# Kernel optimization log

Hardware: AMD Instinct MI355X
Metric: run time of the kernel (lower is better)

Reference implementation:

```python
import jax, jax.numpy as jnp
import numpy as np

N = 100000      # nodes
E = 600000      # edges
IN = 128        # in_dim
HID = 32        # hidden_dim per head (layer 1)
HEADS = 4       # num_heads (layer 1)
NEG_SLOPE = 0.2 # PyG GATConv default negative_slope


def setup_inputs() -> dict:
    key = jax.random.key(0)
    ks = jax.random.split(key, 10)
    x = jax.random.normal(ks[0], (N, IN), dtype=jnp.float32)
    edge_index = jax.random.randint(ks[1], (2, E), 0, N, dtype=jnp.int64)
    # layer 1 params: W1 [IN, HEADS*HID], attention vectors [HEADS, HID], bias [HEADS*HID]
    W1 = jax.random.normal(ks[2], (IN, HEADS * HID), dtype=jnp.float32) / np.float32(np.sqrt(IN))
    att_src1 = jax.random.normal(ks[3], (HEADS, HID), dtype=jnp.float32) * 0.1
    att_dst1 = jax.random.normal(ks[4], (HEADS, HID), dtype=jnp.float32) * 0.1
    b1 = jnp.zeros((HEADS * HID,), dtype=jnp.float32)
    # layer 2 params: heads=1, out channels=1, concat=False
    W2 = jax.random.normal(ks[5], (HEADS * HID, 1), dtype=jnp.float32) / np.float32(np.sqrt(HEADS * HID))
    att_src2 = jax.random.normal(ks[6], (1, 1), dtype=jnp.float32) * 0.1
    att_dst2 = jax.random.normal(ks[7], (1, 1), dtype=jnp.float32) * 0.1
    b2 = jnp.zeros((1,), dtype=jnp.float32)
    return {"x": x, "edge_index": edge_index, "W1": W1, "att_src1": att_src1,
            "att_dst1": att_dst1, "b1": b1, "W2": W2, "att_src2": att_src2,
            "att_dst2": att_dst2, "b2": b2}


def gat_layer(x, src, dst, W, a_src, a_dst, b, heads, ch, concat):
    """PyG GATConv (eval mode): edge score + segment softmax + scatter aggregate."""
    n = x.shape[0]
    h = (x @ W).reshape(n, heads, ch)                    # [N,H,C]
    e_src = jnp.einsum('nhc,hc->nh', h, a_src)           # alpha_src per node
    e_dst = jnp.einsum('nhc,hc->nh', h, a_dst)           # alpha_dst per node
    e = jax.nn.leaky_relu(e_src[src] + e_dst[dst], NEG_SLOPE)  # [E,H]
    m = jax.ops.segment_max(e, dst, num_segments=n)      # stable softmax per dst
    p = jnp.exp(e - m[dst])
    denom = jax.ops.segment_sum(p, dst, num_segments=n)
    alpha = p / (denom[dst] + 1e-16)                     # [E,H]
    out = jax.ops.segment_sum(alpha[:, :, None] * h[src], dst, num_segments=n)  # [N,H,C]
    out = out.reshape(n, heads * ch) if concat else out.mean(axis=1)
    return out + b


def reference(x, edge_index, W1, att_src1, att_dst1, b1, W2, att_src2, att_dst2, b2):
    n = x.shape[0]
    loops = jnp.arange(n, dtype=edge_index.dtype)        # PyG add_self_loops=True
    src = jnp.concatenate([edge_index[0], loops])
    dst = jnp.concatenate([edge_index[1], loops])
    h1 = gat_layer(x, src, dst, W1, att_src1, att_dst1, b1, HEADS, HID, True)   # [N, HEADS*HID]
    out = gat_layer(h1, src, dst, W2, att_src2, att_dst2, b2, 1, 1, False)      # [N, 1]
    return out
```

## Files before the change

kernel.cpp:

```cpp
#include <hip/hip_runtime.h>
#include <hip/hip_fp16.h>
#include <math.h>

#define N_NODES 100000
#define E_EDGES 600000
#define IN_DIM  128
#define HID     32
#define HEADS   4
#define NEG     0.2f
#define CAP     32

typedef __attribute__((ext_vector_type(8))) _Float16 f16x8;
typedef __attribute__((ext_vector_type(4))) float f32x4;

__device__ __forceinline__ float lrelu(float v) { return v > 0.f ? v : NEG * v; }

#define SWZ(r, byteoff) ((byteoff) ^ (((r) & 7) << 4))


__global__ __launch_bounds__(128) void wprep_kernel(const float* __restrict__ W1,
                                                    const float* __restrict__ as1,
                                                    const float* __restrict__ ad1,
                                                    __half* __restrict__ wtx,
                                                    int* __restrict__ cnt) {
    int tid = blockIdx.x * 128 + threadIdx.x;
    for (int i = tid; i < N_NODES; i += 144 * 128) cnt[i] = 0;

    int b = blockIdx.x;
    int t = threadIdx.x;
    float v;
    if (b < 128) {
        v = W1[t * 128 + b];
    } else if (b < 136) {
        int h = b - 128;
        int hh = h & 3;
        const float* av = (h < 4) ? (as1 + hh * 32) : (ad1 + hh * 32);
        float s = 0.f;
        #pragma unroll 8
        for (int c = 0; c < 32; ++c) s += W1[t * 128 + hh * 32 + c] * av[c];
        v = s;
    } else {
        v = 0.f;
    }
    wtx[b * 128 + t] = __float2half(v);
}


__global__ __launch_bounds__(256) void scatter_kernel(const int* __restrict__ ei,
                                                      int* __restrict__ cnt,
                                                      int* __restrict__ idxb) {
    int e = blockIdx.x * 256 + threadIdx.x;
    if (e < E_EDGES) {
        int d = ei[E_EDGES + e];
        int slot = atomicAdd(&cnt[d], 1);
        if (slot < CAP) idxb[d * CAP + slot] = ei[e];
    }
}


__global__ __launch_bounds__(256) void gemm1_kernel(const float* __restrict__ x,
                                                    const __half* __restrict__ wtx,
                                                    __half* __restrict__ h1h,
                                                    float* __restrict__ aab) {
    __shared__ __half lx[64 * 128];
    __shared__ __half lw[144 * 128];
    int t = threadIdx.x;
    int row0 = blockIdx.x * 64;

    #pragma unroll
    for (int it = 0; it < 9; ++it) {
        int idx = t + it * 256;
        int r = idx >> 4, c = idx & 15;
        uint4 v = ((const uint4*)wtx)[idx];
        *(uint4*)((char*)lw + SWZ(r, r * 256 + c * 16)) = v;
    }
    #pragma unroll
    for (int it = 0; it < 8; ++it) {
        int idx = t + it * 256;
        int r = idx >> 5, c = idx & 31;
        int gr = row0 + r;
        float4 v = make_float4(0.f, 0.f, 0.f, 0.f);
        if (gr < N_NODES) v = ((const float4*)x)[gr * 32 + c];
        union { uint2 u; __half2 h[2]; } pk;
        pk.h[0] = __floats2half2_rn(v.x, v.y);
        pk.h[1] = __floats2half2_rn(v.z, v.w);
        *(uint2*)((char*)lx + SWZ(r, r * 256 + c * 8)) = pk.u;
    }
    __syncthreads();

    int w = t >> 6, lane = t & 63;
    int li = lane & 15, g = lane >> 4;
    int arow = w * 16 + li;

    f16x8 af[4];
    #pragma unroll
    for (int kt = 0; kt < 4; ++kt)
        af[kt] = *(const f16x8*)((const char*)lx + SWZ(arow, arow * 256 + kt * 64 + g * 16));

    f32x4 acc[9];
    #pragma unroll
    for (int ct = 0; ct < 9; ++ct) acc[ct] = (f32x4){0.f, 0.f, 0.f, 0.f};

    #pragma unroll
    for (int ct = 0; ct < 9; ++ct) {
        int n = ct * 16 + li;
        #pragma unroll
        for (int kt = 0; kt < 4; ++kt) {
            f16x8 bf = *(const f16x8*)((const char*)lw + SWZ(n, n * 256 + kt * 64 + g * 16));
            acc[ct] = __builtin_amdgcn_mfma_f32_16x16x32_f16(af[kt], bf, acc[ct], 0, 0, 0);
        }
    }

    int gr0 = row0 + w * 16 + g * 4;
    #pragma unroll
    for (int ct = 0; ct < 8; ++ct) {
        int col = ct * 16 + li;
        #pragma unroll
        for (int q = 0; q < 4; ++q) {
            int gr = gr0 + q;
            if (gr < N_NODES) h1h[gr * 128 + col] = __float2half(acc[ct][q]);
        }
    }
    if (li < 8) {
        #pragma unroll
        for (int q = 0; q < 4; ++q) {
            int gr = gr0 + q;
            if (gr < N_NODES) aab[gr * 8 + li] = acc[8][q];
        }
    }
}


__global__ __launch_bounds__(256) void agg1_kernel(const __half* __restrict__ h1h,
                                                   const float* __restrict__ aab,
                                                   const int* __restrict__ cnt,
                                                   const int* __restrict__ idxb,
                                                   const float* __restrict__ b1,
                                                   const float* __restrict__ W2,
                                                   const float* __restrict__ att_src2,
                                                   const float* __restrict__ att_dst2,
                                                   float* __restrict__ h2,
                                                   float* __restrict__ a2s,
                                                   float* __restrict__ a2d) {
    int tid = threadIdx.x;
    int c = tid & 15;
    int n = blockIdx.x * 16 + (tid >> 4);
    int head = c >> 2;
    int deg = min(cnt[n], CAP);
    const int* nb = idxb + (size_t)n * CAP;
    float adn = aab[n * 8 + 4 + head];

    __half2 acc01 = __half2(0.f, 0.f), acc23 = acc01, acc45 = acc01, acc67 = acc01;
    float den = 0.f;

    int s = (deg > 0) ? nb[0] : 0;
    for (int e = 0; e < deg; ++e) {
        int s_next = nb[e + 1];
        float p = __expf(lrelu(aab[s * 8 + head] + adn));
        __half2 pp = __float2half2_rn(p);
        union { uint4 u; __half2 h[4]; } hv;
        hv.u = *(const uint4*)&h1h[s * 128 + c * 8];
        acc01 = __hfma2(pp, hv.h[0], acc01);
        acc23 = __hfma2(pp, hv.h[1], acc23);
        acc45 = __hfma2(pp, hv.h[2], acc45);
        acc67 = __hfma2(pp, hv.h[3], acc67);
        den += p;
        s = s_next;
    }

    float s0 = __low2float(acc01), s1 = __high2float(acc01);
    float s2 = __low2float(acc23), s3 = __high2float(acc23);
    float s4 = __low2float(acc45), s5 = __high2float(acc45);
    float s6 = __low2float(acc67), s7 = __high2float(acc67);

    {
        float p = __expf(lrelu(aab[n * 8 + head] + adn));
        union { uint4 u; __half2 h[4]; } hv;
        hv.u = *(const uint4*)&h1h[n * 128 + c * 8];
        float2 f0 = __half22float2(hv.h[0]), f1 = __half22float2(hv.h[1]);
        float2 f2 = __half22float2(hv.h[2]), f3 = __half22float2(hv.h[3]);
        s0 += p * f0.x; s1 += p * f0.y; s2 += p * f1.x; s3 += p * f1.y;
        s4 += p * f2.x; s5 += p * f2.y; s6 += p * f3.x; s7 += p * f3.y;
        den += p;
    }

    float inv = 1.f / (den + 1e-16f);
    float4 bv0 = ((const float4*)b1)[c * 2];
    float4 bv1 = ((const float4*)b1)[c * 2 + 1];
    float o0 = s0 * inv + bv0.x, o1 = s1 * inv + bv0.y;
    float o2 = s2 * inv + bv0.z, o3 = s3 * inv + bv0.w;
    float o4 = s4 * inv + bv1.x, o5 = s5 * inv + bv1.y;
    float o6 = s6 * inv + bv1.z, o7 = s7 * inv + bv1.w;

    float4 wv0 = ((const float4*)W2)[c * 2];
    float4 wv1 = ((const float4*)W2)[c * 2 + 1];
    float pp = o0 * wv0.x + o1 * wv0.y + o2 * wv0.z + o3 * wv0.w
             + o4 * wv1.x + o5 * wv1.y + o6 * wv1.z + o7 * wv1.w;
    #pragma unroll
    for (int m = 1; m <= 8; m <<= 1) pp += __shfl_xor(pp, m, 64);
    if (c == 0) {
        h2[n] = pp;
        a2s[n] = pp * att_src2[0];
        a2d[n] = pp * att_dst2[0];
    }
}


__global__ __launch_bounds__(256) void agg2_kernel(const float* __restrict__ h2,
                                                   const float* __restrict__ a2s,
                                                   const float* __restrict__ a2d,
                                                   const int* __restrict__ cnt,
                                                   const int* __restrict__ idxb,
                                                   const float* __restrict__ b2,
                                                   float* __restrict__ out) {
    int n = blockIdx.x * 256 + threadIdx.x;
    if (n >= N_NODES) return;
    float adn = a2d[n];
    int deg = min(cnt[n], CAP);
    const int* nb = idxb + (size_t)n * CAP;
    float num = 0.f, den = 0.f;
    for (int i = 0; i < deg; i += 4) {
        int s[4]; bool val[4]; float as_[4], hs[4];
        #pragma unroll
        for (int j = 0; j < 4; ++j) {
            val[j] = (i + j) < deg;
            s[j] = val[j] ? nb[i + j] : n;
        }
        #pragma unroll
        for (int j = 0; j < 4; ++j) as_[j] = a2s[s[j]];
        #pragma unroll
        for (int j = 0; j < 4; ++j) hs[j] = h2[s[j]];
        #pragma unroll
        for (int j = 0; j < 4; ++j) {
            float p = val[j] ? __expf(lrelu(as_[j] + adn)) : 0.f;
            num += p * hs[j];
            den += p;
        }
    }
    {
        float p = __expf(lrelu(a2s[n] + adn));
        num += p * h2[n];
        den += p;
    }
    out[n] = num / (den + 1e-16f) + b2[0];
}


extern "C" void kernel_launch(void* const* d_in, const int* in_sizes, int n_in,
                              void* d_out, int out_size, void* d_ws, size_t ws_size,
                              hipStream_t stream) {
    const float* x        = (const float*)d_in[0];
    const int*   ei       = (const int*)d_in[1];
    const float* W1       = (const float*)d_in[2];
    const float* att_src1 = (const float*)d_in[3];
    const float* att_dst1 = (const float*)d_in[4];
    const float* b1       = (const float*)d_in[5];
    const float* W2       = (const float*)d_in[6];
    const float* att_src2 = (const float*)d_in[7];
    const float* att_dst2 = (const float*)d_in[8];
    const float* b2       = (const float*)d_in[9];
    float* out = (float*)d_out;

    char* ws = (char*)d_ws;
    size_t off = 0;
    auto alloc = [&](size_t bytes) {
        char* p = ws + off;
        off = (off + bytes + 255) & ~(size_t)255;
        return p;
    };
    __half* h1h    = (__half*)alloc((size_t)N_NODES * 128 * 2);
    float*  aab    = (float*)alloc((size_t)N_NODES * 8 * 4);
    __half* wtx    = (__half*)alloc((size_t)144 * 128 * 2);
    float*  h2     = (float*)alloc((size_t)N_NODES * 4);
    float*  a2s    = (float*)alloc((size_t)N_NODES * 4);
    float*  a2d    = (float*)alloc((size_t)N_NODES * 4);
    int*    cnt    = (int*)alloc((size_t)N_NODES * 4);
    int*    idxb   = (int*)alloc(((size_t)N_NODES * CAP + 64) * 4);

    const int NB_NODE = (N_NODES + 255) / 256;
    const int NB_EDGE = (E_EDGES + 255) / 256;
    const int NB_AGG1 = N_NODES / 16;
    const int NB_GEMM = (N_NODES + 63) / 64;

    wprep_kernel<<<144, 128, 0, stream>>>(W1, att_src1, att_dst1, wtx, cnt);
    scatter_kernel<<<NB_EDGE, 256, 0, stream>>>(ei, cnt, idxb);
    gemm1_kernel<<<NB_GEMM, 256, 0, stream>>>(x, wtx, h1h, aab);
    agg1_kernel<<<NB_AGG1, 256, 0, stream>>>(h1h, aab, cnt, idxb,
                                             b1, W2, att_src2, att_dst2,
                                             h2, a2s, a2d);
    agg2_kernel<<<NB_NODE, 256, 0, stream>>>(h2, a2s, a2d, cnt, idxb, b2, out);
}
```

Before: 191.8 us.

## Fuse edge scatter into GEMM launch and pack layer-2 node data as float4

The edge-bucketing scatter runs as extra blocks of the GEMM kernel instead of a separate launch, so the memory-bound atomics can overlap with GEMM compute and one launch is removed. Layer-2 per-node values (h2, alpha_src, alpha_dst) are packed into one float4 array so agg2 does a single 16-byte gather per neighbour instead of two scalar gathers. In exchange, scatter blocks reserve the GEMM's large shared-memory allocation, which may limit how many fit per CU, and the packed array moves more bytes per node.

```diff
diff --git a/kernel.cpp b/kernel.cpp
--- a/kernel.cpp
+++ b/kernel.cpp
@@ -9,6 +9,7 @@
 #define HEADS   4
 #define NEG     0.2f
 #define CAP     32
+#define NB_GEMM_C 1563
 
 typedef __attribute__((ext_vector_type(8))) _Float16 f16x8;
 typedef __attribute__((ext_vector_type(4))) float f32x4;
@@ -46,25 +47,27 @@
 }
 
 
-__global__ __launch_bounds__(256) void scatter_kernel(const int* __restrict__ ei,
-                                                      int* __restrict__ cnt,
-                                                      int* __restrict__ idxb) {
-    int e = blockIdx.x * 256 + threadIdx.x;
-    if (e < E_EDGES) {
-        int d = ei[E_EDGES + e];
-        int slot = atomicAdd(&cnt[d], 1);
-        if (slot < CAP) idxb[d * CAP + slot] = ei[e];
-    }
-}
-
-
-__global__ __launch_bounds__(256) void gemm1_kernel(const float* __restrict__ x,
+__global__ __launch_bounds__(256) void gemsc_kernel(const float* __restrict__ x,
                                                     const __half* __restrict__ wtx,
                                                     __half* __restrict__ h1h,
-                                                    float* __restrict__ aab) {
+                                                    float* __restrict__ aab,
+                                                    const int* __restrict__ ei,
+                                                    int* __restrict__ cnt,
+                                                    int* __restrict__ idxb) {
     __shared__ __half lx[64 * 128];
     __shared__ __half lw[144 * 128];
     int t = threadIdx.x;
+
+    if (blockIdx.x >= NB_GEMM_C) {
+        int e = (blockIdx.x - NB_GEMM_C) * 256 + t;
+        if (e < E_EDGES) {
+            int d = ei[E_EDGES + e];
+            int slot = atomicAdd(&cnt[d], 1);
+            if (slot < CAP) idxb[d * CAP + slot] = ei[e];
+        }
+        return;
+    }
+
     int row0 = blockIdx.x * 64;
 
     #pragma unroll
@@ -139,9 +142,7 @@
                                                    const float* __restrict__ W2,
                                                    const float* __restrict__ att_src2,
                                                    const float* __restrict__ att_dst2,
-                                                   float* __restrict__ h2,
-                                                   float* __restrict__ a2s,
-                                                   float* __restrict__ a2d) {
+                                                   float4* __restrict__ pk2) {
     int tid = threadIdx.x;
     int c = tid & 15;
     int n = blockIdx.x * 16 + (tid >> 4);
@@ -199,47 +200,42 @@
     #pragma unroll
     for (int m = 1; m <= 8; m <<= 1) pp += __shfl_xor(pp, m, 64);
     if (c == 0) {
-        h2[n] = pp;
-        a2s[n] = pp * att_src2[0];
-        a2d[n] = pp * att_dst2[0];
-    }
-}
-
-
-__global__ __launch_bounds__(256) void agg2_kernel(const float* __restrict__ h2,
-                                                   const float* __restrict__ a2s,
-                                                   const float* __restrict__ a2d,
+        pk2[n] = make_float4(pp, pp * att_src2[0], pp * att_dst2[0], 0.f);
+    }
+}
+
+
+__global__ __launch_bounds__(256) void agg2_kernel(const float4* __restrict__ pk2,
                                                    const int* __restrict__ cnt,
                                                    const int* __restrict__ idxb,
                                                    const float* __restrict__ b2,
                                                    float* __restrict__ out) {
     int n = blockIdx.x * 256 + threadIdx.x;
     if (n >= N_NODES) return;
-    float adn = a2d[n];
+    float4 me = pk2[n];
+    float adn = me.z;
     int deg = min(cnt[n], CAP);
     const int* nb = idxb + (size_t)n * CAP;
     float num = 0.f, den = 0.f;
     for (int i = 0; i < deg; i += 4) {
-        int s[4]; bool val[4]; float as_[4], hs[4];
+        int s[4]; bool val[4]; float4 ps[4];
         #pragma unroll
         for (int j = 0; j < 4; ++j) {
             val[j] = (i + j) < deg;
             s[j] = val[j] ? nb[i + j] : n;
         }
         #pragma unroll
-        for (int j = 0; j < 4; ++j) as_[j] = a2s[s[j]];
-        #pragma unroll
-        for (int j = 0; j < 4; ++j) hs[j] = h2[s[j]];
+        for (int j = 0; j < 4; ++j) ps[j] = pk2[s[j]];
         #pragma unroll
         for (int j = 0; j < 4; ++j) {
-            float p = val[j] ? __expf(lrelu(as_[j] + adn)) : 0.f;
-            num += p * hs[j];
+            float p = val[j] ? __expf(lrelu(ps[j].y + adn)) : 0.f;
+            num += p * ps[j].x;
             den += p;
         }
     }
     {
-        float p = __expf(lrelu(a2s[n] + adn));
-        num += p * h2[n];
+        float p = __expf(lrelu(me.y + adn));
+        num += p * me.x;
         den += p;
     }
     out[n] = num / (den + 1e-16f) + b2[0];
@@ -271,22 +267,18 @@
     __half* h1h    = (__half*)alloc((size_t)N_NODES * 128 * 2);
     float*  aab    = (float*)alloc((size_t)N_NODES * 8 * 4);
     __half* wtx    = (__half*)alloc((size_t)144 * 128 * 2);
-    float*  h2     = (float*)alloc((size_t)N_NODES * 4);
-    float*  a2s    = (float*)alloc((size_t)N_NODES * 4);
-    float*  a2d    = (float*)alloc((size_t)N_NODES * 4);
+    float4* pk2    = (float4*)alloc((size_t)N_NODES * 16);
     int*    cnt    = (int*)alloc((size_t)N_NODES * 4);
     int*    idxb   = (int*)alloc(((size_t)N_NODES * CAP + 64) * 4);
 
     const int NB_NODE = (N_NODES + 255) / 256;
     const int NB_EDGE = (E_EDGES + 255) / 256;
     const int NB_AGG1 = N_NODES / 16;
-    const int NB_GEMM = (N_NODES + 63) / 64;
 
     wprep_kernel<<<144, 128, 0, stream>>>(W1, att_src1, att_dst1, wtx, cnt);
-    scatter_kernel<<<NB_EDGE, 256, 0, stream>>>(ei, cnt, idxb);
-    gemm1_kernel<<<NB_GEMM, 256, 0, stream>>>(x, wtx, h1h, aab);
+    gemsc_kernel<<<NB_GEMM_C + NB_EDGE, 256, 0, stream>>>(x, wtx, h1h, aab,
+                                                          ei, cnt, idxb);
     agg1_kernel<<<NB_AGG1, 256, 0, stream>>>(h1h, aab, cnt, idxb,
-                                             b1, W2, att_src2, att_dst2,
-                                             h2, a2s, a2d);
-    agg2_kernel<<<NB_NODE, 256, 0, stream>>>(h2, a2s, a2d, cnt, idxb, b2, out);
-}
+                                             b1, W2, att_src2, att_dst2, pk2);
+    agg2_kernel<<<NB_NODE, 256, 0, stream>>>(pk2, cnt, idxb, b2, out);
+}
```

Result: slower. 202.5 us (+5.6%).
